# Kernel optimization log

Measured on AMD Instinct MI355X. Metric: run time of the kernel, lower is better.

Reference implementation:

```python
import jax, jax.numpy as jnp
import numpy as np

B, S, H = 4, 2048, 2048      # batch, seq, hidden_size
E, K, F = 8, 2, 1408         # n_routed_experts, topk, moe_inter_dim


def setup_inputs() -> dict:
    key = jax.random.key(0)
    k0, k1, k2, k3, k4 = jax.random.split(key, 5)
    s = 0.02  # init scale for weights
    return {
        "hidden_states": jax.random.normal(k0, (B, S, H), dtype=jnp.float32),
        "router_w": jax.random.normal(k1, (E, H), dtype=jnp.float32) * s,
        "gate_w": jax.random.normal(k2, (E, F, H), dtype=jnp.float32) * s,
        "up_w": jax.random.normal(k3, (E, F, H), dtype=jnp.float32) * s,
        "down_w": jax.random.normal(k4, (E, H, F), dtype=jnp.float32) * s,
    }


def reference(hidden_states, router_w, gate_w, up_w, down_w):
    shape = hidden_states.shape
    x = hidden_states.reshape(-1, H)                  # [T, H], T = B*S
    # Router: softmax over all experts, then top-k of the probabilities
    logits = x @ router_w.T                            # [T, E]
    weights = jax.nn.softmax(logits, axis=-1)          # [T, E]
    topk_weight, indices = jax.lax.top_k(weights, K)   # [T, K]
    # normalize_top_k_affinities
    topk_weight = topk_weight / (topk_weight.sum(axis=-1, keepdims=True) + 1e-20)
    # Per-token per-expert combine weight: [T, E]
    combine = jnp.einsum("tk,tke->te", topk_weight,
                         jax.nn.one_hot(indices, E, dtype=topk_weight.dtype))
    # Experts: swiglu MLP, weighted-combined. Loop over the small fixed set of experts.
    out = jnp.zeros_like(x)
    for e in range(E):
        h = jax.nn.silu(x @ gate_w[e].T) * (x @ up_w[e].T)  # [T, F]
        out = out + combine[:, e:e + 1] * (h @ down_w[e].T)  # [T, H]
    return out.reshape(shape)
```

## Files before the change

kernel.cpp:

```cpp
#include <hip/hip_runtime.h>
#include <stdint.h>

#define T_TOK 8192
#define HD 2048
#define NE 8
#define FD 1408
#define BM 128
#define BN 128
#define BK 64
#define MAXT 136
#define ROWS_CAP 17408

typedef unsigned short u16;
typedef __attribute__((ext_vector_type(8))) short bf16x8;
typedef __attribute__((ext_vector_type(4))) float f32x4;

__device__ __forceinline__ u16 f2bf(float f) {
  unsigned u = __float_as_uint(f);
  unsigned r = (u + 0x7fffu + ((u >> 16) & 1u)) >> 16;
  return (u16)r;
}
__device__ __forceinline__ float bflo(unsigned u) { return __uint_as_float(u << 16); }
__device__ __forceinline__ float bfhi(unsigned u) { return __uint_as_float(u & 0xffff0000u); }

__device__ __forceinline__ void async_copy16(const void* g, void* l) {
  __builtin_amdgcn_global_load_lds(
      (__attribute__((address_space(1))) void*)(uintptr_t)g,
      (__attribute__((address_space(3))) void*)(uintptr_t)l,
      16, 0, 0);
}

__global__ void k_convert_w(const float* __restrict__ gw, const float* __restrict__ uw,
                            const float* __restrict__ dw, u16* __restrict__ gwb,
                            u16* __restrict__ uwb, u16* __restrict__ dwb) {
  const long n_w = (long)NE * FD * HD / 4;
  const float* s; u16* d;
  if (blockIdx.y == 0)      { s = gw; d = gwb; }
  else if (blockIdx.y == 1) { s = uw; d = uwb; }
  else                      { s = dw; d = dwb; }
  long stride = (long)gridDim.x * blockDim.x;
  for (long j = (long)blockIdx.x * blockDim.x + threadIdx.x; j < n_w; j += stride) {
    float4 v = ((const float4*)s)[j];
    ushort4 o;
    o.x = f2bf(v.x); o.y = f2bf(v.y); o.z = f2bf(v.z); o.w = f2bf(v.w);
    ((ushort4*)d)[j] = o;
  }
}

__global__ __launch_bounds__(256) void k_router(
    const float* __restrict__ x, const float* __restrict__ rw, u16* __restrict__ xb,
    int* __restrict__ topk_idx, float* __restrict__ topk_w)
{
  int t = blockIdx.x;
  int tid = threadIdx.x;
  int lane = tid & 63;
  int wave = tid >> 6;
  const float4* xr = (const float4*)(x + (size_t)t * HD);
  const float4* w0 = (const float4*)(rw + (size_t)(wave * 2) * HD);
  const float4* w1 = (const float4*)(rw + (size_t)(wave * 2 + 1) * HD);
  float a0 = 0.f, a1 = 0.f;
  for (int i = lane; i < HD / 4; i += 64) {
    float4 xv = xr[i], v0 = w0[i], v1 = w1[i];
    a0 += xv.x * v0.x + xv.y * v0.y + xv.z * v0.z + xv.w * v0.w;
    a1 += xv.x * v1.x + xv.y * v1.y + xv.z * v1.z + xv.w * v1.w;
  }
  {
    float4 v0 = xr[tid * 2], v1 = xr[tid * 2 + 1];
    uint4 o;
    o.x = (unsigned)f2bf(v0.x) | ((unsigned)f2bf(v0.y) << 16);
    o.y = (unsigned)f2bf(v0.z) | ((unsigned)f2bf(v0.w) << 16);
    o.z = (unsigned)f2bf(v1.x) | ((unsigned)f2bf(v1.y) << 16);
    o.w = (unsigned)f2bf(v1.z) | ((unsigned)f2bf(v1.w) << 16);
    ((uint4*)(xb + (size_t)t * HD))[tid] = o;
  }
#pragma unroll
  for (int off = 32; off > 0; off >>= 1) {
    a0 += __shfl_down(a0, off);
    a1 += __shfl_down(a1, off);
  }
  __shared__ float lg[NE];
  if (lane == 0) { lg[wave * 2] = a0; lg[wave * 2 + 1] = a1; }
  __syncthreads();
  if (tid == 0) {
    float m1 = lg[0], m2 = -3.4e38f;
    int i1 = 0, i2 = 0;
    for (int e = 1; e < NE; e++) {
      float v = lg[e];
      if (v > m1)      { m2 = m1; i2 = i1; m1 = v; i1 = e; }
      else if (v > m2) { m2 = v; i2 = e; }
    }
    float wA = 1.f / (1.f + expf(m2 - m1));
    float wB = 1.f - wA;
    topk_idx[t * 2] = i1; topk_idx[t * 2 + 1] = i2;
    topk_w[t * 2] = wA;   topk_w[t * 2 + 1] = wB;
  }
}

__global__ __launch_bounds__(256) void k_meta(const int* __restrict__ topk_idx,
                                              int* __restrict__ meta,
                                              int* __restrict__ row_token) {
  __shared__ int hist[NE];
  __shared__ int tstart[NE + 1];
  __shared__ int roff[NE];
  int tid = threadIdx.x;
  if (tid < NE) hist[tid] = 0;
  for (int i = tid; i < ROWS_CAP; i += 256) row_token[i] = 0;
  __syncthreads();
  int cnt[NE] = {};
  for (int i = tid; i < 2 * T_TOK; i += 256) {
    int v = topk_idx[i];
#pragma unroll
    for (int e = 0; e < NE; e++) cnt[e] += (v == e);
  }
#pragma unroll
  for (int e = 0; e < NE; e++) if (cnt[e]) atomicAdd(&hist[e], cnt[e]);
  __syncthreads();
  if (tid == 0) {
    int off = 0, nt = 0;
    for (int e = 0; e < NE; e++) {
      int tiles = (hist[e] + BM - 1) / BM;
      roff[e] = off;
      tstart[e] = nt;
      nt += tiles;
      off += tiles * BM;
    }
    tstart[NE] = nt;
  }
  __syncthreads();
  int nt = tstart[NE];
  if (tid < NE) meta[16 + tid] = roff[tid];
  if (tid == 0) meta[8] = nt;
  if (tid < nt) {
    int e = 0;
#pragma unroll
    for (int k = 1; k < NE; k++) e += (tid >= tstart[k]);
    meta[64 + tid] = e;
    meta[256 + tid] = roff[e] + (tid - tstart[e]) * BM;
  }
}

__global__ __launch_bounds__(256) void k_scatter(const int* __restrict__ topk_idx,
                                                 int* __restrict__ meta,
                                                 int* __restrict__ row_token,
                                                 int* __restrict__ tokrow) {
  __shared__ int hist[NE], base[NE];
  int tid = threadIdx.x;
  if (tid < NE) hist[tid] = 0;
  __syncthreads();
  int t = blockIdx.x * 256 + tid;
  int e0 = topk_idx[t * 2], e1 = topk_idx[t * 2 + 1];
  int r0 = atomicAdd(&hist[e0], 1);
  int r1 = atomicAdd(&hist[e1], 1);
  __syncthreads();
  if (tid < NE) base[tid] = atomicAdd(&meta[16 + tid], hist[tid]);
  __syncthreads();
  int p0 = base[e0] + r0, p1 = base[e1] + r1;
  row_token[p0] = t; tokrow[t * 2] = p0;
  row_token[p1] = t; tokrow[t * 2 + 1] = p1;
}

__global__ __launch_bounds__(256, 2) void k_gemm1(
    const u16* __restrict__ xb, const u16* __restrict__ gwb, const u16* __restrict__ uwb,
    const int* __restrict__ meta, const int* __restrict__ row_token, u16* __restrict__ hb)
{
  int total = meta[8];
  int tile = blockIdx.x;
  if (tile >= total) return;
  int e = meta[64 + tile];
  int row0 = meta[256 + tile];
  int ntile = blockIdx.y;

  __shared__ u16 As[BM * BK];
  __shared__ u16 Bg[BN * BK];
  __shared__ u16 Bu[BN * BK];

  int lane = threadIdx.x & 63;
  int wave = threadIdx.x >> 6;
  int wr = wave >> 1, wc = wave & 1;

  const u16* aG[4]; const u16* gG[4]; const u16* uG[4];
  unsigned ldsOff[4];
#pragma unroll
  for (int j = 0; j < 4; j++) {
    int r = wave * 32 + j * 8 + (lane >> 3);
    int c = (lane & 7) ^ (r & 7);
    int tok = row_token[row0 + r];
    aG[j] = xb + (size_t)tok * HD + c * 8;
    int nrow = ntile * BN + r;
    size_t wof = ((size_t)e * FD + nrow) * HD + c * 8;
    gG[j] = gwb + wof;
    uG[j] = uwb + wof;
    ldsOff[j] = (unsigned)(wave * 32 + j * 8) * 128;
  }

  f32x4 accG[4][4] = {};
  f32x4 accU[4][4] = {};

  for (int kt = 0; kt < HD / BK; kt++) {
    int ko = kt * BK;
#pragma unroll
    for (int j = 0; j < 4; j++) async_copy16(aG[j] + ko, (char*)As + ldsOff[j]);
#pragma unroll
    for (int j = 0; j < 4; j++) async_copy16(gG[j] + ko, (char*)Bg + ldsOff[j]);
#pragma unroll
    for (int j = 0; j < 4; j++) async_copy16(uG[j] + ko, (char*)Bu + ldsOff[j]);
    __syncthreads();
#pragma unroll
    for (int kk = 0; kk < 2; kk++) {
      bf16x8 av[4], gv[4], uv[4];
#pragma unroll
      for (int mi = 0; mi < 4; mi++) {
        int r = wr * 64 + mi * 16 + (lane & 15);
        int slot = (kk * 4 + (lane >> 4)) ^ (r & 7);
        av[mi] = *(const bf16x8*)((const char*)As + (unsigned)(r * 8 + slot) * 16);
      }
#pragma unroll
      for (int ni = 0; ni < 4; ni++) {
        int r = wc * 64 + ni * 16 + (lane & 15);
        int slot = (kk * 4 + (lane >> 4)) ^ (r & 7);
        gv[ni] = *(const bf16x8*)((const char*)Bg + (unsigned)(r * 8 + slot) * 16);
        uv[ni] = *(const bf16x8*)((const char*)Bu + (unsigned)(r * 8 + slot) * 16);
      }
#pragma unroll
      for (int mi = 0; mi < 4; mi++)
#pragma unroll
        for (int ni = 0; ni < 4; ni++) {
          accG[mi][ni] = __builtin_amdgcn_mfma_f32_16x16x32_bf16(av[mi], gv[ni], accG[mi][ni], 0, 0, 0);
          accU[mi][ni] = __builtin_amdgcn_mfma_f32_16x16x32_bf16(av[mi], uv[ni], accU[mi][ni], 0, 0, 0);
        }
    }
    __syncthreads();
  }

#pragma unroll
  for (int mi = 0; mi < 4; mi++) {
#pragma unroll
    for (int r = 0; r < 4; r++) {
      int row = row0 + wr * 64 + mi * 16 + (lane >> 4) * 4 + r;
      u16* hrow = hb + (size_t)row * FD + ntile * BN + wc * 64 + (lane & 15);
#pragma unroll
      for (int ni = 0; ni < 4; ni++) {
        float g = accG[mi][ni][r];
        float u = accU[mi][ni][r];
        float s = g / (1.f + __expf(-g));
        hrow[ni * 16] = f2bf(s * u);
      }
    }
  }
}

__global__ __launch_bounds__(256, 4) void k_gemm2(
    const u16* __restrict__ hb, const u16* __restrict__ dwb,
    const int* __restrict__ meta, u16* __restrict__ Y)
{
  int total = meta[8];
  int tile = blockIdx.x;
  if (tile >= total) return;
  int e = meta[64 + tile];
  int row0 = meta[256 + tile];
  int ntile = blockIdx.y;

  __shared__ u16 As[BM * BK];
  __shared__ u16 Bs[BN * BK];

  int lane = threadIdx.x & 63;
  int wave = threadIdx.x >> 6;
  int wr = wave >> 1, wc = wave & 1;

  const u16* aG[4]; const u16* bG[4];
  unsigned ldsOff[4];
#pragma unroll
  for (int j = 0; j < 4; j++) {
    int r = wave * 32 + j * 8 + (lane >> 3);
    int c = (lane & 7) ^ (r & 7);
    aG[j] = hb + (size_t)(row0 + r) * FD + c * 8;
    int nrow = ntile * BN + r;
    bG[j] = dwb + ((size_t)e * HD + nrow) * FD + c * 8;
    ldsOff[j] = (unsigned)(wave * 32 + j * 8) * 128;
  }

  f32x4 acc[4][4] = {};

  for (int kt = 0; kt < FD / BK; kt++) {
    int ko = kt * BK;
#pragma unroll
    for (int j = 0; j < 4; j++) async_copy16(aG[j] + ko, (char*)As + ldsOff[j]);
#pragma unroll
    for (int j = 0; j < 4; j++) async_copy16(bG[j] + ko, (char*)Bs + ldsOff[j]);
    __syncthreads();
#pragma unroll
    for (int kk = 0; kk < 2; kk++) {
      bf16x8 av[4], bv[4];
#pragma unroll
      for (int mi = 0; mi < 4; mi++) {
        int r = wr * 64 + mi * 16 + (lane & 15);
        int slot = (kk * 4 + (lane >> 4)) ^ (r & 7);
        av[mi] = *(const bf16x8*)((const char*)As + (unsigned)(r * 8 + slot) * 16);
      }
#pragma unroll
      for (int ni = 0; ni < 4; ni++) {
        int r = wc * 64 + ni * 16 + (lane & 15);
        int slot = (kk * 4 + (lane >> 4)) ^ (r & 7);
        bv[ni] = *(const bf16x8*)((const char*)Bs + (unsigned)(r * 8 + slot) * 16);
      }
#pragma unroll
      for (int mi = 0; mi < 4; mi++)
#pragma unroll
        for (int ni = 0; ni < 4; ni++)
          acc[mi][ni] = __builtin_amdgcn_mfma_f32_16x16x32_bf16(av[mi], bv[ni], acc[mi][ni], 0, 0, 0);
    }
    __syncthreads();
  }

#pragma unroll
  for (int mi = 0; mi < 4; mi++) {
#pragma unroll
    for (int r = 0; r < 4; r++) {
      int grow = row0 + wr * 64 + mi * 16 + (lane >> 4) * 4 + r;
      u16* yrow = Y + (size_t)grow * HD + ntile * BN + wc * 64 + (lane & 15);
#pragma unroll
      for (int ni = 0; ni < 4; ni++)
        yrow[ni * 16] = f2bf(acc[mi][ni][r]);
    }
  }
}

__global__ __launch_bounds__(256) void k_combine(
    const u16* __restrict__ Y, const int* __restrict__ tokrow,
    const float* __restrict__ topk_w, float* __restrict__ out)
{
  int t = blockIdx.x;
  int i = threadIdx.x;
  int rA = tokrow[t * 2], rB = tokrow[t * 2 + 1];
  float wA = topk_w[t * 2], wB = topk_w[t * 2 + 1];
  uint4 a = *(const uint4*)(Y + (size_t)rA * HD + i * 8);
  uint4 b = *(const uint4*)(Y + (size_t)rB * HD + i * 8);
  float4 o0, o1;
  o0.x = wA * bflo(a.x) + wB * bflo(b.x);
  o0.y = wA * bfhi(a.x) + wB * bfhi(b.x);
  o0.z = wA * bflo(a.y) + wB * bflo(b.y);
  o0.w = wA * bfhi(a.y) + wB * bfhi(b.y);
  o1.x = wA * bflo(a.z) + wB * bflo(b.z);
  o1.y = wA * bfhi(a.z) + wB * bfhi(b.z);
  o1.z = wA * bflo(a.w) + wB * bflo(b.w);
  o1.w = wA * bfhi(a.w) + wB * bfhi(b.w);
  float* op = out + (size_t)t * HD + i * 8;
  *(float4*)op = o0;
  *(float4*)(op + 4) = o1;
}

extern "C" void kernel_launch(void* const* d_in, const int* in_sizes, int n_in,
                              void* d_out, int out_size, void* d_ws, size_t ws_size,
                              hipStream_t stream) {
  const float* x  = (const float*)d_in[0];
  const float* rw = (const float*)d_in[1];
  const float* gw = (const float*)d_in[2];
  const float* uw = (const float*)d_in[3];
  const float* dw = (const float*)d_in[4];
  float* out = (float*)d_out;

  char* w = (char*)d_ws;
  int*   meta      = (int*)w;
  int*   row_token = (int*)(w + 4096);
  int*   topk_idx  = (int*)(w + 4096 + ROWS_CAP * 4);
  float* topk_w    = (float*)(w + 4096 + ROWS_CAP * 4 + T_TOK * 2 * 4);
  int*   tokrow    = (int*)(w + 4096 + ROWS_CAP * 4 + T_TOK * 4 * 4);
  size_t off = (size_t)1 << 20;
  u16* xb  = (u16*)(w + off); off += (size_t)T_TOK * HD * 2;
  u16* gwb = (u16*)(w + off); off += (size_t)NE * FD * HD * 2;
  u16* uwb = (u16*)(w + off); off += (size_t)NE * FD * HD * 2;
  u16* dwb = (u16*)(w + off); off += (size_t)NE * HD * FD * 2;
  u16* hb  = (u16*)(w + off);
  u16* Y = xb;

  k_convert_w<<<dim3(4096, 3), 256, 0, stream>>>(gw, uw, dw, gwb, uwb, dwb);

  k_router<<<T_TOK, 256, 0, stream>>>(x, rw, xb, topk_idx, topk_w);
  k_meta<<<1, 256, 0, stream>>>(topk_idx, meta, row_token);
  k_scatter<<<T_TOK / 256, 256, 0, stream>>>(topk_idx, meta, row_token, tokrow);

  k_gemm1<<<dim3(MAXT, FD / BN), 256, 0, stream>>>(xb, gwb, uwb, meta, row_token, hb);
  k_gemm2<<<dim3(MAXT, HD / BN), 256, 0, stream>>>(hb, dwb, meta, Y);
  k_combine<<<T_TOK, 256, 0, stream>>>(Y, tokrow, topk_w, out);
}
```

Before: 746.6 us.

## Fuse weight conversion into router and merge meta/scatter into one scan kernel

Folds the fp32-to-bf16 weight conversion into the router kernel's grid, removing a separate launch. Replaces the histogram and atomic scatter kernels with a single-block kernel that does a per-expert prefix scan and deterministic scatter. Also lowers gemm2 occupancy hint from 4 to 3 blocks per CU. The single-block scatter serializes 16K writes across 256 threads, which may be slower than the multi-block scatter it replaces.

Result: faster. 724.6 us (-2.9%).

```diff
diff --git a/kernel.cpp b/kernel.cpp
--- a/kernel.cpp
+++ b/kernel.cpp
@@ -30,25 +30,17 @@
       16, 0, 0);
 }
 
-__global__ void k_convert_w(const float* __restrict__ gw, const float* __restrict__ uw,
-                            const float* __restrict__ dw, u16* __restrict__ gwb,
-                            u16* __restrict__ uwb, u16* __restrict__ dwb) {
-  const long n_w = (long)NE * FD * HD / 4;
-  const float* s; u16* d;
-  if (blockIdx.y == 0)      { s = gw; d = gwb; }
-  else if (blockIdx.y == 1) { s = uw; d = uwb; }
-  else                      { s = dw; d = dwb; }
-  long stride = (long)gridDim.x * blockDim.x;
-  for (long j = (long)blockIdx.x * blockDim.x + threadIdx.x; j < n_w; j += stride) {
-    float4 v = ((const float4*)s)[j];
-    ushort4 o;
-    o.x = f2bf(v.x); o.y = f2bf(v.y); o.z = f2bf(v.z); o.w = f2bf(v.w);
-    ((ushort4*)d)[j] = o;
-  }
+__device__ __forceinline__ void conv4(const float* __restrict__ s, u16* __restrict__ d, long j) {
+  float4 v = ((const float4*)s)[j];
+  ushort4 o;
+  o.x = f2bf(v.x); o.y = f2bf(v.y); o.z = f2bf(v.z); o.w = f2bf(v.w);
+  ((ushort4*)d)[j] = o;
 }
 
 __global__ __launch_bounds__(256) void k_router(
-    const float* __restrict__ x, const float* __restrict__ rw, u16* __restrict__ xb,
+    const float* __restrict__ x, const float* __restrict__ rw,
+    const float* __restrict__ gw, const float* __restrict__ uw, const float* __restrict__ dw,
+    u16* __restrict__ xb, u16* __restrict__ gwb, u16* __restrict__ uwb, u16* __restrict__ dwb,
     int* __restrict__ topk_idx, float* __restrict__ topk_w)
 {
   int t = blockIdx.x;
@@ -94,42 +86,59 @@
     topk_idx[t * 2] = i1; topk_idx[t * 2 + 1] = i2;
     topk_w[t * 2] = wA;   topk_w[t * 2 + 1] = wB;
   }
-}
-
-__global__ __launch_bounds__(256) void k_meta(const int* __restrict__ topk_idx,
-                                              int* __restrict__ meta,
-                                              int* __restrict__ row_token) {
-  __shared__ int hist[NE];
-  __shared__ int tstart[NE + 1];
-  __shared__ int roff[NE];
+  const long n_w = (long)NE * FD * HD / 4;
+  const long gstride = (long)gridDim.x * 256;
+  const long g0 = (long)t * 256 + tid;
+  for (long j = g0; j < n_w; j += gstride) conv4(gw, gwb, j);
+  for (long j = g0; j < n_w; j += gstride) conv4(uw, uwb, j);
+  for (long j = g0; j < n_w; j += gstride) conv4(dw, dwb, j);
+}
+
+__global__ __launch_bounds__(256) void k_meta_scatter(
+    const int* __restrict__ topk_idx, int* __restrict__ meta,
+    int* __restrict__ row_token, int* __restrict__ tokrow)
+{
+  __shared__ int scan[NE][257];
+  __shared__ int roff[NE], tstart[NE + 1];
   int tid = threadIdx.x;
-  if (tid < NE) hist[tid] = 0;
   for (int i = tid; i < ROWS_CAP; i += 256) row_token[i] = 0;
+  if (tid < NE) scan[tid][0] = 0;
+  int cnt[NE] = {};
+  int base_i = tid * 64;
+#pragma unroll 4
+  for (int j = 0; j < 64; j++) {
+    int v = topk_idx[base_i + j];
+#pragma unroll
+    for (int e = 0; e < NE; e++) cnt[e] += (v == e);
+  }
+  int i = tid + 1;
+#pragma unroll
+  for (int e = 0; e < NE; e++) scan[e][i] = cnt[e];
   __syncthreads();
-  int cnt[NE] = {};
-  for (int i = tid; i < 2 * T_TOK; i += 256) {
-    int v = topk_idx[i];
-#pragma unroll
-    for (int e = 0; e < NE; e++) cnt[e] += (v == e);
-  }
-#pragma unroll
-  for (int e = 0; e < NE; e++) if (cnt[e]) atomicAdd(&hist[e], cnt[e]);
-  __syncthreads();
+  for (int s = 1; s < 256; s <<= 1) {
+    int add[NE];
+#pragma unroll
+    for (int e = 0; e < NE; e++) add[e] = (i >= s) ? scan[e][i - s] : 0;
+    __syncthreads();
+#pragma unroll
+    for (int e = 0; e < NE; e++) scan[e][i] += add[e];
+    __syncthreads();
+  }
   if (tid == 0) {
     int off = 0, nt = 0;
     for (int e = 0; e < NE; e++) {
-      int tiles = (hist[e] + BM - 1) / BM;
+      int tot = scan[e][256];
+      int tiles = (tot + BM - 1) / BM;
       roff[e] = off;
       tstart[e] = nt;
       nt += tiles;
       off += tiles * BM;
     }
     tstart[NE] = nt;
+    meta[8] = nt;
   }
   __syncthreads();
   int nt = tstart[NE];
-  if (tid < NE) meta[16 + tid] = roff[tid];
-  if (tid == 0) meta[8] = nt;
   if (tid < nt) {
     int e = 0;
 #pragma unroll
@@ -137,26 +146,18 @@
     meta[64 + tid] = e;
     meta[256 + tid] = roff[e] + (tid - tstart[e]) * BM;
   }
-}
-
-__global__ __launch_bounds__(256) void k_scatter(const int* __restrict__ topk_idx,
-                                                 int* __restrict__ meta,
-                                                 int* __restrict__ row_token,
-                                                 int* __restrict__ tokrow) {
-  __shared__ int hist[NE], base[NE];
-  int tid = threadIdx.x;
-  if (tid < NE) hist[tid] = 0;
-  __syncthreads();
-  int t = blockIdx.x * 256 + tid;
-  int e0 = topk_idx[t * 2], e1 = topk_idx[t * 2 + 1];
-  int r0 = atomicAdd(&hist[e0], 1);
-  int r1 = atomicAdd(&hist[e1], 1);
-  __syncthreads();
-  if (tid < NE) base[tid] = atomicAdd(&meta[16 + tid], hist[tid]);
-  __syncthreads();
-  int p0 = base[e0] + r0, p1 = base[e1] + r1;
-  row_token[p0] = t; tokrow[t * 2] = p0;
-  row_token[p1] = t; tokrow[t * 2 + 1] = p1;
+  int pos[NE];
+#pragma unroll
+  for (int e = 0; e < NE; e++) pos[e] = roff[e] + scan[e][tid];
+  for (int j = 0; j < 64; j++) {
+    int idx = base_i + j;
+    int v = topk_idx[idx];
+    int p = 0;
+#pragma unroll
+    for (int e = 0; e < NE; e++) if (v == e) p = pos[e]++;
+    row_token[p] = idx >> 1;
+    tokrow[idx] = p;
+  }
 }
 
 __global__ __launch_bounds__(256, 2) void k_gemm1(
@@ -249,7 +250,7 @@
   }
 }
 
-__global__ __launch_bounds__(256, 4) void k_gemm2(
+__global__ __launch_bounds__(256, 3) void k_gemm2(
     const u16* __restrict__ hb, const u16* __restrict__ dwb,
     const int* __restrict__ meta, u16* __restrict__ Y)
 {
@@ -373,12 +374,8 @@
   u16* hb  = (u16*)(w + off);
   u16* Y = xb;
 
-  k_convert_w<<<dim3(4096, 3), 256, 0, stream>>>(gw, uw, dw, gwb, uwb, dwb);
-
-  k_router<<<T_TOK, 256, 0, stream>>>(x, rw, xb, topk_idx, topk_w);
-  k_meta<<<1, 256, 0, stream>>>(topk_idx, meta, row_token);
-  k_scatter<<<T_TOK / 256, 256, 0, stream>>>(topk_idx, meta, row_token, tokrow);
-
+  k_router<<<T_TOK, 256, 0, stream>>>(x, rw, gw, uw, dw, xb, gwb, uwb, dwb, topk_idx, topk_w);
+  k_meta_scatter<<<1, 256, 0, stream>>>(topk_idx, meta, row_token, tokrow);
   k_gemm1<<<dim3(MAXT, FD / BN), 256, 0, stream>>>(xb, gwb, uwb, meta, row_token, hb);
   k_gemm2<<<dim3(MAXT, HD / BN), 256, 0, stream>>>(hb, dwb, meta, Y);
   k_combine<<<T_TOK, 256, 0, stream>>>(Y, tokrow, topk_w, out);
```
